# Kernel tuning notes

Measured on AMD Instinct MI355X. Metric: run time of the kernel, lower is better.

## Reference

```python
import jax, jax.numpy as jnp
import numpy as np

T, N, G, H, COV, TW, E = 96, 1024, 128, 512, 8, 8, 32768
D2 = TW * (TW - 1)          # 56, GNN summary width
IN = COV + D2               # 64, exogenous input width


def setup_inputs() -> dict:
    key = jax.random.key(0)
    ks = jax.random.split(key, 32)
    s = 1.0 / np.sqrt(H)

    def u(k, shape):
        return jax.random.uniform(k, shape, jnp.float32, -s, s)

    inp = {
        "input": jax.random.normal(ks[0], (T, 1, IN), jnp.float32),
        "x_nodes": jax.random.normal(ks[1], (T, N, N), jnp.float32),
        "edge_index": jax.random.randint(ks[2], (T, 2, E), 0, N, dtype=jnp.int64),
        "W1": u(ks[3], (N, G)), "b1": u(ks[4], (G,)),
        "W2": u(ks[5], (G, G)), "b2": u(ks[6], (G,)),
        "Wfc": u(ks[7], (G * N, D2)), "bfc": u(ks[8], (D2,)),
        "W_ii": u(ks[9], (IN, H)), "W_gi": u(ks[10], (D2, H)), "W_hi": u(ks[11], (H, H)), "b_i": u(ks[12], (H,)),
        "W_if": u(ks[13], (IN, H)), "W_gf": u(ks[14], (D2, H)), "W_hf": u(ks[15], (H, H)), "b_f": u(ks[16], (H,)),
        "W_ig": u(ks[17], (IN, H)), "W_gg": u(ks[18], (D2, H)), "W_hg": u(ks[19], (H, H)), "b_g": u(ks[20], (H,)),
        "W_io": u(ks[21], (IN, H)), "W_go": u(ks[22], (D2, H)), "W_ho": u(ks[23], (H, H)), "b_o": u(ks[24], (H,)),
    }
    return inp


def reference(input, x_nodes, edge_index,
              W1, b1, W2, b2, Wfc, bfc,
              W_ii, W_gi, W_hi, b_i,
              W_if, W_gf, W_hf, b_f,
              W_ig, W_gg, W_hg, b_g,
              W_io, W_go, W_ho, b_o):
    self_loops = jnp.arange(N, dtype=edge_index.dtype)

    def gcn_conv(x, src, dst, dinv, W, b):
        # GCNConv: out[dst] += d^-1/2[src] d^-1/2[dst] * (x @ W)[src], plus bias
        xw = x @ W                                   # [N, F_out]
        norm = dinv[src] * dinv[dst]                 # [E+N]
        msg = xw[src] * norm[:, None]
        return jax.ops.segment_sum(msg, dst, num_segments=N) + b

    def step(carry, inputs):
        h, c = carry
        x_t, xg, ei = inputs                         # [1,IN], [N,N], [2,E]
        src = jnp.concatenate([ei[0], self_loops])   # add self-loops
        dst = jnp.concatenate([ei[1], self_loops])
        deg = jax.ops.segment_sum(jnp.ones(src.shape, jnp.float32), dst, num_segments=N)
        dinv = jnp.where(deg > 0, jax.lax.rsqrt(jnp.maximum(deg, 1.0)), 0.0)

        xh = jax.nn.relu(gcn_conv(xg, src, dst, dinv, W1, b1))
        xh = gcn_conv(xh, src, dst, dinv, W2, b2)    # [N, G]
        g = jax.nn.relu(xh.reshape(1, -1) @ Wfc + bfc)  # [1, D2]

        i = jax.nn.sigmoid(x_t @ W_ii + g @ W_gi + h @ W_hi + b_i)
        f = jax.nn.sigmoid(x_t @ W_if + g @ W_gf + h @ W_hf + b_f)
        gt = jnp.tanh(x_t @ W_ig + g @ W_gg + h @ W_hg + b_g)
        o = jax.nn.sigmoid(x_t @ W_io + g @ W_go + h @ W_ho + b_o)
        c = f * c + i * gt
        h = o * jnp.tanh(c)
        return (h, c), h

    h0 = jnp.zeros((1, H), jnp.float32)
    c0 = jnp.zeros((1, H), jnp.float32)
    (h, c), outputs = jax.lax.scan(step, (h0, c0), (input, x_nodes, edge_index))
    return outputs, h, c
```

## Files before the change

### kernel.cpp

```cpp
#include <hip/hip_runtime.h>
#include <stdint.h>

#define T_    96
#define TC_   32
#define N_    1024
#define G_    128
#define H_    512
#define E_    32768
#define EN_   33792
#define D2_   56
#define IN_   64
#define KFC_  131072

typedef __bf16 bf16_t;
typedef __bf16 bf16x8 __attribute__((ext_vector_type(8)));
typedef float  f32x4  __attribute__((ext_vector_type(4)));
typedef unsigned short u16;
typedef unsigned long long u64;

struct PtrQuadF { const float* p[4]; };

__device__ inline bf16x8 cvt8(const float* p) {
    const f32x4 a0 = *(const f32x4*)p;
    const f32x4 a1 = *(const f32x4*)(p + 4);
    bf16x8 r;
    r[0] = (bf16_t)a0[0]; r[1] = (bf16_t)a0[1]; r[2] = (bf16_t)a0[2]; r[3] = (bf16_t)a0[3];
    r[4] = (bf16_t)a1[0]; r[5] = (bf16_t)a1[1]; r[6] = (bf16_t)a1[2]; r[7] = (bf16_t)a1[3];
    return r;
}


__global__ __launch_bounds__(256) void deg_kernel(const int* __restrict__ ei, int* __restrict__ deg) {
    int t = blockIdx.y;
    int idx = blockIdx.x * 256 + threadIdx.x;
    if (idx >= EN_) return;
    int d = (idx < E_) ? ei[(size_t)t * 2 * E_ + E_ + idx] : (idx - E_);
    atomicAdd(&deg[t * N_ + d], 1);
}

__global__ __launch_bounds__(1024) void scan_kernel(const int* __restrict__ deg, int* __restrict__ rowptr,
                                                    int* __restrict__ fill, float* __restrict__ dinv) {
    int t = blockIdx.x, i = threadIdx.x;
    __shared__ int a[N_], b[N_];
    int d = deg[t * N_ + i];
    a[i] = d;
    __syncthreads();
    int* cur = a; int* nxt = b;
    for (int off = 1; off < N_; off <<= 1) {
        int v = cur[i];
        if (i >= off) v += cur[i - off];
        nxt[i] = v;
        __syncthreads();
        int* tmp = cur; cur = nxt; nxt = tmp;
    }
    int incl = cur[i];
    int start = incl - d + t * EN_;
    rowptr[t * N_ + i] = start;
    fill[t * N_ + i] = start;
    dinv[t * N_ + i] = rsqrtf((float)d);
}

__global__ __launch_bounds__(256) void fill_kernel(const int* __restrict__ ei, int* __restrict__ fill,
                                                   u16* __restrict__ colv) {
    int t = blockIdx.y;
    int idx = blockIdx.x * 256 + threadIdx.x;
    if (idx >= EN_) return;
    int s, d;
    if (idx < E_) {
        s = ei[(size_t)t * 2 * E_ + idx];
        d = ei[(size_t)t * 2 * E_ + E_ + idx];
    } else {
        s = d = idx - E_;
    }
    int pos = atomicAdd(&fill[t * N_ + d], 1);
    colv[pos] = (u16)s;
}


__global__ __launch_bounds__(256) void densify_kernel(const int* __restrict__ rowptr, const int* __restrict__ deg,
                                                      const u16* __restrict__ colv, const float* __restrict__ dinv,
                                                      bf16_t* __restrict__ S, int t0) {
    int tl = blockIdx.y;
    int t = t0 + tl;
    int w = threadIdx.x >> 6, l = threadIdx.x & 63;
    int r = blockIdx.x * 4 + w;
    __shared__ float rowbuf[4][N_];
    for (int i = l; i < N_; i += 64) rowbuf[w][i] = 0.f;
    __syncthreads();
    int start = rowptr[t * N_ + r];
    int n = deg[t * N_ + r];
    float dr = dinv[t * N_ + r];
    for (int e = l; e < n; e += 64) {
        int c = colv[start + e];
        atomicAdd(&rowbuf[w][c], dinv[t * N_ + c] * dr);
    }
    __syncthreads();
    bf16_t* dst = S + ((size_t)tl * N_ + r) * N_;
    for (int i = l; i < N_; i += 64) dst[i] = (bf16_t)rowbuf[w][i];
}


__global__ __launch_bounds__(256) void transpose_kernel(const float* __restrict__ src, bf16_t* __restrict__ dst,
                                                        int R, int C, int Cpad) {
    __shared__ bf16_t tile[64][65];
    int rb = blockIdx.x * 64, cb = blockIdx.y * 64;
    int tx = threadIdx.x & 63, ty = threadIdx.x >> 6;
#pragma unroll
    for (int i = 0; i < 16; i++) {
        int r = rb + ty * 16 + i;
        int c = cb + tx;
        float v = 0.f;
        if (r < R && c < C) v = src[(size_t)r * C + c];
        tile[ty * 16 + i][tx] = (bf16_t)v;
    }
    __syncthreads();
#pragma unroll
    for (int i = 0; i < 16; i++) {
        int c = cb + ty * 16 + i;
        int r = rb + tx;
        if (c < Cpad && r < R) dst[(size_t)c * R + r] = tile[tx][ty * 16 + i];
    }
}


__global__ __launch_bounds__(256) void whcvt_kernel(PtrQuadF Wh, bf16_t* __restrict__ dst) {
    int g = blockIdx.y;
    int idx = blockIdx.x * 256 + threadIdx.x;
    dst[(size_t)g * H_ * H_ + idx] = (bf16_t)Wh.p[g][idx];
}


template<bool BF32>
__global__ __launch_bounds__(256) void gemm_g(const bf16_t* __restrict__ A, const void* __restrict__ Bp,
                                              bf16_t* __restrict__ C, const float* __restrict__ bias, int relu,
                                              int K, int Mtiles, size_t sA, size_t sB, size_t sC, int ldc) {
    int t = blockIdx.y;
    int mi = blockIdx.x % Mtiles, ni = blockIdx.x / Mtiles;
    int tid = threadIdx.x;
    int w = tid >> 6, l = tid & 63;
    int wm = w & 1, wn = w >> 1;
    int lm = l & 15, lq = l >> 4;
    f32x4 acc[4][4] = {};
    const bf16_t* Ab = A + sA * t + (size_t)(mi * 128 + wm * 64 + lm) * K + lq * 8;
    size_t bO = sB * t + (size_t)(ni * 128 + wn * 64 + lm) * K + lq * 8;
    const bf16_t* Bb16 = (const bf16_t*)Bp + bO;
    const float*  Bb32 = (const float*)Bp + bO;
    for (int k0 = 0; k0 < K; k0 += 32) {
        bf16x8 af[4], bfv[4];
#pragma unroll
        for (int i = 0; i < 4; i++) af[i] = *(const bf16x8*)(Ab + (size_t)i * 16 * K + k0);
#pragma unroll
        for (int i = 0; i < 4; i++) {
            if (BF32) bfv[i] = cvt8(Bb32 + (size_t)i * 16 * K + k0);
            else      bfv[i] = *(const bf16x8*)(Bb16 + (size_t)i * 16 * K + k0);
        }
#pragma unroll
        for (int mt = 0; mt < 4; mt++)
#pragma unroll
            for (int nt = 0; nt < 4; nt++)
                acc[mt][nt] = __builtin_amdgcn_mfma_f32_16x16x32_bf16(af[mt], bfv[nt], acc[mt][nt], 0, 0, 0);
    }
#pragma unroll
    for (int mt = 0; mt < 4; mt++)
#pragma unroll
        for (int nt = 0; nt < 4; nt++) {
            int colg = ni * 128 + wn * 64 + nt * 16 + lm;
            float bv = bias ? bias[colg] : 0.f;
#pragma unroll
            for (int r = 0; r < 4; r++) {
                int row = mi * 128 + wm * 64 + mt * 16 + lq * 4 + r;
                float v = acc[mt][nt][r] + bv;
                if (relu) v = fmaxf(v, 0.f);
                C[sC * t + (size_t)row * ldc + colg] = (bf16_t)v;
            }
        }
}


__global__ __launch_bounds__(256) void gfc_kernel(const bf16_t* __restrict__ XH2, const bf16_t* __restrict__ WfcT,
                                                  float* __restrict__ g_acc, int t0) {
    int tid = threadIdx.x;
    int w = tid >> 6, l = tid & 63;
    int lm = l & 15, lq = l >> 4;
    int n = w * 16 + lm;
    size_t k0 = (size_t)blockIdx.x * 1024;
    f32x4 acc[2] = {};
    const bf16_t* Ab = XH2 + (size_t)lm * KFC_ + k0 + lq * 8;
    const bf16_t* Bb = WfcT + (size_t)n * KFC_ + k0 + lq * 8;
    for (int ks = 0; ks < 32; ks++) {
        bf16x8 bfr = *(const bf16x8*)(Bb + ks * 32);
        bf16x8 a0  = *(const bf16x8*)(Ab + ks * 32);
        bf16x8 a1  = *(const bf16x8*)(Ab + (size_t)16 * KFC_ + ks * 32);
        acc[0] = __builtin_amdgcn_mfma_f32_16x16x32_bf16(a0, bfr, acc[0], 0, 0, 0);
        acc[1] = __builtin_amdgcn_mfma_f32_16x16x32_bf16(a1, bfr, acc[1], 0, 0, 0);
    }
#pragma unroll
    for (int mt = 0; mt < 2; mt++)
#pragma unroll
        for (int r = 0; r < 4; r++) {
            int t = t0 + mt * 16 + lq * 4 + r;
            if (n < D2_) atomicAdd(&g_acc[t * 64 + n], acc[mt][r]);
        }
}


__global__ __launch_bounds__(512) void pregate_kernel(const float* __restrict__ xin, const float* __restrict__ g_acc,
                                                      const float* __restrict__ bfc,
                                                      PtrQuadF Wi, PtrQuadF Wg, PtrQuadF Wb,
                                                      float* __restrict__ out) {
    int gate = blockIdx.x, t = blockIdx.y, j = threadIdx.x;
    __shared__ float gl[D2_];
    __shared__ float xl[IN_];
    if (j < D2_) gl[j] = fmaxf(g_acc[t * 64 + j] + bfc[j], 0.f);
    if (j < IN_) xl[j] = xin[t * IN_ + j];
    __syncthreads();
    const float* wi = Wi.p[gate];
    const float* wg = Wg.p[gate];
    float acc = Wb.p[gate][j];
#pragma unroll 4
    for (int k = 0; k < IN_; k++) acc += xl[k] * wi[k * H_ + j];
#pragma unroll 4
    for (int k = 0; k < D2_; k++) acc += gl[k] * wg[k * H_ + j];
    out[(t * 4 + gate) * H_ + j] = acc;
}


__global__ __launch_bounds__(256) void lstm_kernel(const bf16_t* __restrict__ Whb, const float* __restrict__ pregate,
                                                   u64* __restrict__ h_slot, float* __restrict__ out) {
    int tid = threadIdx.x, bid = blockIdx.x;
    int jl = tid >> 3, kc = tid & 7;
    int j = bid * 32 + jl;
    int k0 = kc * 64;

    uint32_t w[128];
#pragma unroll
    for (int g4 = 0; g4 < 4; g4++) {
        const bf16_t* W = Whb + (size_t)g4 * H_ * H_;
#pragma unroll
        for (int m = 0; m < 32; m++) {
            int k = k0 + 2 * m;
            uint32_t lo = *(const u16*)(W + (size_t)k * H_ + j);
            uint32_t hi = *(const u16*)(W + (size_t)(k + 1) * H_ + j);
            w[g4 * 32 + m] = lo | (hi << 16);
        }
    }

    __shared__ __align__(16) float hl[H_];
    hl[tid] = 0.f;
    hl[tid + 256] = 0.f;
    float c = 0.f;
    __syncthreads();

    for (int step = 0; step < 96; step++) {
        float p0 = 0.f, p1 = 0.f, p2 = 0.f, p3 = 0.f;
        if (kc == 0) {
            const float* pre = pregate + (size_t)step * (4 * H_);
            p0 = pre[0 * H_ + j]; p1 = pre[1 * H_ + j];
            p2 = pre[2 * H_ + j]; p3 = pre[3 * H_ + j];
        }

        float s0 = 0.f, s1 = 0.f, s2 = 0.f, s3 = 0.f;
        const float4* h4 = (const float4*)(hl + k0);
#pragma unroll
        for (int q = 0; q < 16; q++) {
            float4 hq = h4[q];
#pragma unroll
            for (int p = 0; p < 2; p++) {
                float h0 = p ? hq.z : hq.x;
                float h1 = p ? hq.w : hq.y;
                int mi = q * 2 + p;
                uint32_t wv;
                wv = w[0 * 32 + mi];
                s0 += __uint_as_float(wv << 16) * h0 + __uint_as_float(wv & 0xffff0000u) * h1;
                wv = w[1 * 32 + mi];
                s1 += __uint_as_float(wv << 16) * h0 + __uint_as_float(wv & 0xffff0000u) * h1;
                wv = w[2 * 32 + mi];
                s2 += __uint_as_float(wv << 16) * h0 + __uint_as_float(wv & 0xffff0000u) * h1;
                wv = w[3 * 32 + mi];
                s3 += __uint_as_float(wv << 16) * h0 + __uint_as_float(wv & 0xffff0000u) * h1;
            }
        }
        s0 += __shfl_xor(s0, 1); s0 += __shfl_xor(s0, 2); s0 += __shfl_xor(s0, 4);
        s1 += __shfl_xor(s1, 1); s1 += __shfl_xor(s1, 2); s1 += __shfl_xor(s1, 4);
        s2 += __shfl_xor(s2, 1); s2 += __shfl_xor(s2, 2); s2 += __shfl_xor(s2, 4);
        s3 += __shfl_xor(s3, 1); s3 += __shfl_xor(s3, 2); s3 += __shfl_xor(s3, 4);

        if (kc == 0) {
            float ig = 1.f / (1.f + __expf(-(s0 + p0)));
            float fg = 1.f / (1.f + __expf(-(s1 + p1)));
            float gg = tanhf(s2 + p2);
            float og = 1.f / (1.f + __expf(-(s3 + p3)));
            c = fg * c + ig * gg;
            float h = og * tanhf(c);
            if (step < 95) {
                u64 v = ((u64)(unsigned int)(step + 1) << 32) | (u64)__float_as_uint(h);
                __hip_atomic_store(&h_slot[(size_t)step * H_ + j], v, __ATOMIC_RELAXED, __HIP_MEMORY_SCOPE_AGENT);
            }
            out[step * H_ + j] = h;
            if (step == 95) {
                out[96 * H_ + j] = h;
                out[97 * H_ + j] = c;
            }
        }
        if (step < 95) {
            __syncthreads();
            if (tid < 64) {
                unsigned int want = (unsigned int)(step + 1);
                const u64* base = h_slot + (size_t)step * H_ + tid * 8;
                u64 v[8];
                int need = 0xff;
                while (need) {
#pragma unroll
                    for (int s = 0; s < 8; s++)
                        if (need & (1 << s))
                            v[s] = __hip_atomic_load(&base[s], __ATOMIC_RELAXED, __HIP_MEMORY_SCOPE_AGENT);
                    int nd = 0;
#pragma unroll
                    for (int s = 0; s < 8; s++)
                        if ((need & (1 << s)) && (unsigned int)(v[s] >> 32) != want) nd |= 1 << s;
                    need = nd;
                    if (need) __builtin_amdgcn_s_sleep(1);
                }
                float4 f0, f1;
                f0.x = __uint_as_float((unsigned int)v[0]); f0.y = __uint_as_float((unsigned int)v[1]);
                f0.z = __uint_as_float((unsigned int)v[2]); f0.w = __uint_as_float((unsigned int)v[3]);
                f1.x = __uint_as_float((unsigned int)v[4]); f1.y = __uint_as_float((unsigned int)v[5]);
                f1.z = __uint_as_float((unsigned int)v[6]); f1.w = __uint_as_float((unsigned int)v[7]);
                ((float4*)hl)[tid * 2] = f0;
                ((float4*)hl)[tid * 2 + 1] = f1;
            }
            __syncthreads();
        }
    }
}


extern "C" void kernel_launch(void* const* d_in, const int* in_sizes, int n_in,
                              void* d_out, int out_size, void* d_ws, size_t ws_size,
                              hipStream_t stream) {
    const float* xin    = (const float*)d_in[0];
    const float* xnodes = (const float*)d_in[1];
    const int*   ei     = (const int*)d_in[2];
    const float* W1  = (const float*)d_in[3];
    const float* b1  = (const float*)d_in[4];
    const float* W2  = (const float*)d_in[5];
    const float* b2  = (const float*)d_in[6];
    const float* Wfc = (const float*)d_in[7];
    const float* bfc = (const float*)d_in[8];

    PtrQuadF Wi = {{(const float*)d_in[9],  (const float*)d_in[13], (const float*)d_in[17], (const float*)d_in[21]}};
    PtrQuadF Wg = {{(const float*)d_in[10], (const float*)d_in[14], (const float*)d_in[18], (const float*)d_in[22]}};
    PtrQuadF Wh = {{(const float*)d_in[11], (const float*)d_in[15], (const float*)d_in[19], (const float*)d_in[23]}};
    PtrQuadF Wb = {{(const float*)d_in[12], (const float*)d_in[16], (const float*)d_in[20], (const float*)d_in[24]}};

    char* ws = (char*)d_ws;
    size_t off = 0;
    auto alloc = [&](size_t bytes) { void* p = ws + off; off += (bytes + 255) & ~(size_t)255; return p; };

    bf16_t* S       = (bf16_t*)alloc((size_t)TC_ * N_ * N_ * 2);
    bf16_t* C1T     = (bf16_t*)alloc((size_t)TC_ * 128 * N_ * 2);
    bf16_t* XH1     = (bf16_t*)alloc((size_t)TC_ * N_ * 128 * 2);
    bf16_t* C2T     = (bf16_t*)alloc((size_t)TC_ * 128 * N_ * 2);
    u16*    colv    = (u16*)   alloc((size_t)T_ * EN_ * 2);
    int*    deg     = (int*)   alloc((size_t)T_ * N_ * 4);
    int*    rowptr  = (int*)   alloc((size_t)T_ * N_ * 4);
    int*    fillp   = (int*)   alloc((size_t)T_ * N_ * 4);
    float*  dinv    = (float*) alloc((size_t)T_ * N_ * 4);
    bf16_t* W1t     = (bf16_t*)alloc((size_t)128 * 1024 * 2);
    bf16_t* W2t     = (bf16_t*)alloc((size_t)128 * 128 * 2);
    bf16_t* WfcT    = (bf16_t*)alloc((size_t)64 * KFC_ * 2);
    bf16_t* Whb     = (bf16_t*)alloc((size_t)4 * H_ * H_ * 2);
    float*  g_acc   = (float*) alloc((size_t)T_ * 64 * 4);
    float*  pregate = (float*) alloc((size_t)T_ * 4 * H_ * 4);
    u64*    h_slot  = (u64*)   alloc((size_t)T_ * H_ * 8);
    bf16_t* XH2     = C1T;

    hipMemsetAsync(deg, 0, (size_t)T_ * N_ * 4, stream);
    hipMemsetAsync(g_acc, 0, (size_t)T_ * 64 * 4, stream);

    deg_kernel<<<dim3(132, T_), 256, 0, stream>>>(ei, deg);
    scan_kernel<<<T_, 1024, 0, stream>>>(deg, rowptr, fillp, dinv);
    fill_kernel<<<dim3(132, T_), 256, 0, stream>>>(ei, fillp, colv);

    transpose_kernel<<<dim3(16, 2), 256, 0, stream>>>(W1, W1t, 1024, 128, 128);
    transpose_kernel<<<dim3(2, 2), 256, 0, stream>>>(W2, W2t, 128, 128, 128);
    transpose_kernel<<<dim3(2048, 1), 256, 0, stream>>>(Wfc, WfcT, KFC_, D2_, 64);
    whcvt_kernel<<<dim3(1024, 4), 256, 0, stream>>>(Wh, Whb);

    for (int c = 0; c < T_ / TC_; c++) {
        int t0 = c * TC_;
        densify_kernel<<<dim3(256, TC_), 256, 0, stream>>>(rowptr, deg, colv, dinv, S, t0);
        gemm_g<true><<<dim3(8, TC_), 256, 0, stream>>>(
            W1t, xnodes + (size_t)t0 * N_ * N_, C1T, nullptr, 0,
            1024, 1, 0, (size_t)N_ * N_, (size_t)128 * N_, N_);
        gemm_g<false><<<dim3(8, TC_), 256, 0, stream>>>(
            S, C1T, XH1, b1, 1,
            1024, 8, (size_t)N_ * N_, (size_t)128 * N_, (size_t)N_ * 128, 128);
        gemm_g<false><<<dim3(8, TC_), 256, 0, stream>>>(
            W2t, XH1, C2T, nullptr, 0,
            128, 1, 0, (size_t)N_ * 128, (size_t)128 * N_, N_);
        gemm_g<false><<<dim3(8, TC_), 256, 0, stream>>>(
            S, C2T, XH2, b2, 0,
            1024, 8, (size_t)N_ * N_, (size_t)128 * N_, (size_t)N_ * 128, 128);
        gfc_kernel<<<128, 256, 0, stream>>>(XH2, WfcT, g_acc, t0);
    }

    pregate_kernel<<<dim3(4, T_), 512, 0, stream>>>(xin, g_acc, bfc, Wi, Wg, Wb, pregate);

    lstm_kernel<<<16, 256, 0, stream>>>(Whb, pregate, h_slot, (float*)d_out);
}
```

Measured before the change: 1.622 ms.

## Replace dense normalized adjacency GEMMs with CSR sparse aggregation

```diff
diff --git a/kernel.cpp b/kernel.cpp
--- a/kernel.cpp
+++ b/kernel.cpp
@@ -61,7 +61,7 @@
 }
 
 __global__ __launch_bounds__(256) void fill_kernel(const int* __restrict__ ei, int* __restrict__ fill,
-                                                   u16* __restrict__ colv) {
+                                                   const float* __restrict__ dinv, u64* __restrict__ ecv) {
     int t = blockIdx.y;
     int idx = blockIdx.x * 256 + threadIdx.x;
     if (idx >= EN_) return;
@@ -72,31 +72,9 @@
     } else {
         s = d = idx - E_;
     }
+    float nrm = dinv[t * N_ + s] * dinv[t * N_ + d];
     int pos = atomicAdd(&fill[t * N_ + d], 1);
-    colv[pos] = (u16)s;
-}
-
-
-__global__ __launch_bounds__(256) void densify_kernel(const int* __restrict__ rowptr, const int* __restrict__ deg,
-                                                      const u16* __restrict__ colv, const float* __restrict__ dinv,
-                                                      bf16_t* __restrict__ S, int t0) {
-    int tl = blockIdx.y;
-    int t = t0 + tl;
-    int w = threadIdx.x >> 6, l = threadIdx.x & 63;
-    int r = blockIdx.x * 4 + w;
-    __shared__ float rowbuf[4][N_];
-    for (int i = l; i < N_; i += 64) rowbuf[w][i] = 0.f;
-    __syncthreads();
-    int start = rowptr[t * N_ + r];
-    int n = deg[t * N_ + r];
-    float dr = dinv[t * N_ + r];
-    for (int e = l; e < n; e += 64) {
-        int c = colv[start + e];
-        atomicAdd(&rowbuf[w][c], dinv[t * N_ + c] * dr);
-    }
-    __syncthreads();
-    bf16_t* dst = S + ((size_t)tl * N_ + r) * N_;
-    for (int i = l; i < N_; i += 64) dst[i] = (bf16_t)rowbuf[w][i];
+    ecv[pos] = ((u64)__float_as_uint(nrm) << 32) | (unsigned int)s;
 }
 
 
@@ -120,6 +98,23 @@
         int r = rb + tx;
         if (c < Cpad && r < R) dst[(size_t)c * R + r] = tile[tx][ty * 16 + i];
     }
+}
+
+
+__global__ __launch_bounds__(256) void transpose16_kernel(const bf16_t* __restrict__ src, bf16_t* __restrict__ dst) {
+    __shared__ bf16_t tile[64][65];
+    int tl = blockIdx.z;
+    const bf16_t* s = src + (size_t)tl * 128 * N_;
+    bf16_t* d = dst + (size_t)tl * N_ * 128;
+    int rb = blockIdx.y * 64, cb = blockIdx.x * 64;
+    int tx = threadIdx.x & 63, ty = threadIdx.x >> 6;
+#pragma unroll
+    for (int i = 0; i < 16; i++)
+        tile[ty * 16 + i][tx] = s[(size_t)(rb + ty * 16 + i) * N_ + cb + tx];
+    __syncthreads();
+#pragma unroll
+    for (int i = 0; i < 16; i++)
+        d[(size_t)(cb + ty * 16 + i) * 128 + rb + tx] = tile[tx][ty * 16 + i];
 }
 
 
@@ -174,6 +169,43 @@
                 C[sC * t + (size_t)row * ldc + colg] = (bf16_t)v;
             }
         }
+}
+
+
+__device__ inline void spmm_acc(u64 q, const bf16_t* Fb, int l, float& a0, float& a1) {
+    int c = (int)(unsigned int)q;
+    float wn = __uint_as_float((unsigned int)(q >> 32));
+    unsigned int pk = *(const unsigned int*)(Fb + (size_t)c * 128 + 2 * l);
+    a0 += wn * __uint_as_float(pk << 16);
+    a1 += wn * __uint_as_float(pk & 0xffff0000u);
+}
+
+__global__ __launch_bounds__(256) void spmm_kernel(const int* __restrict__ rowptr, const int* __restrict__ deg,
+                                                   const u64* __restrict__ ecv, const bf16_t* __restrict__ F,
+                                                   const float* __restrict__ bias, int relu,
+                                                   bf16_t* __restrict__ out, int t0) {
+    int tl = blockIdx.y, t = t0 + tl;
+    int w = threadIdx.x >> 6, l = threadIdx.x & 63;
+    int r = blockIdx.x * 4 + w;
+    int start = rowptr[t * N_ + r];
+    int n = deg[t * N_ + r];
+    const bf16_t* Fb = F + (size_t)tl * N_ * 128;
+    const u64* ep = ecv + start;
+    float a0 = 0.f, a1 = 0.f;
+    int e = 0;
+    for (; e + 4 <= n; e += 4) {
+        u64 q0 = ep[e], q1 = ep[e + 1], q2 = ep[e + 2], q3 = ep[e + 3];
+        spmm_acc(q0, Fb, l, a0, a1);
+        spmm_acc(q1, Fb, l, a0, a1);
+        spmm_acc(q2, Fb, l, a0, a1);
+        spmm_acc(q3, Fb, l, a0, a1);
+    }
+    for (; e < n; e++) spmm_acc(ep[e], Fb, l, a0, a1);
+    float v0 = a0 + bias[2 * l], v1 = a1 + bias[2 * l + 1];
+    if (relu) { v0 = fmaxf(v0, 0.f); v1 = fmaxf(v1, 0.f); }
+    bf16_t b0 = (bf16_t)v0, b1 = (bf16_t)v1;
+    unsigned int po = (unsigned int)*(u16*)&b0 | ((unsigned int)*(u16*)&b1 << 16);
+    *(unsigned int*)((u16*)(out + ((size_t)tl * N_ + r) * 128) + 2 * l) = po;
 }
 
 
@@ -357,11 +389,12 @@
     size_t off = 0;
     auto alloc = [&](size_t bytes) { void* p = ws + off; off += (bytes + 255) & ~(size_t)255; return p; };
 
-    bf16_t* S       = (bf16_t*)alloc((size_t)TC_ * N_ * N_ * 2);
     bf16_t* C1T     = (bf16_t*)alloc((size_t)TC_ * 128 * N_ * 2);
+    bf16_t* C1      = (bf16_t*)alloc((size_t)TC_ * N_ * 128 * 2);
     bf16_t* XH1     = (bf16_t*)alloc((size_t)TC_ * N_ * 128 * 2);
-    bf16_t* C2T     = (bf16_t*)alloc((size_t)TC_ * 128 * N_ * 2);
-    u16*    colv    = (u16*)   alloc((size_t)T_ * EN_ * 2);
+    bf16_t* C2      = (bf16_t*)alloc((size_t)TC_ * N_ * 128 * 2);
+    bf16_t* XH2     = (bf16_t*)alloc((size_t)TC_ * N_ * 128 * 2);
+    u64*    ecv     = (u64*)   alloc((size_t)T_ * EN_ * 8);
     int*    deg     = (int*)   alloc((size_t)T_ * N_ * 4);
     int*    rowptr  = (int*)   alloc((size_t)T_ * N_ * 4);
     int*    fillp   = (int*)   alloc((size_t)T_ * N_ * 4);
@@ -373,14 +406,13 @@
     float*  g_acc   = (float*) alloc((size_t)T_ * 64 * 4);
     float*  pregate = (float*) alloc((size_t)T_ * 4 * H_ * 4);
     u64*    h_slot  = (u64*)   alloc((size_t)T_ * H_ * 8);
-    bf16_t* XH2     = C1T;
 
     hipMemsetAsync(deg, 0, (size_t)T_ * N_ * 4, stream);
     hipMemsetAsync(g_acc, 0, (size_t)T_ * 64 * 4, stream);
 
     deg_kernel<<<dim3(132, T_), 256, 0, stream>>>(ei, deg);
     scan_kernel<<<T_, 1024, 0, stream>>>(deg, rowptr, fillp, dinv);
-    fill_kernel<<<dim3(132, T_), 256, 0, stream>>>(ei, fillp, colv);
+    fill_kernel<<<dim3(132, T_), 256, 0, stream>>>(ei, fillp, dinv, ecv);
 
     transpose_kernel<<<dim3(16, 2), 256, 0, stream>>>(W1, W1t, 1024, 128, 128);
     transpose_kernel<<<dim3(2, 2), 256, 0, stream>>>(W2, W2t, 128, 128, 128);
@@ -389,19 +421,15 @@
 
     for (int c = 0; c < T_ / TC_; c++) {
         int t0 = c * TC_;
-        densify_kernel<<<dim3(256, TC_), 256, 0, stream>>>(rowptr, deg, colv, dinv, S, t0);
         gemm_g<true><<<dim3(8, TC_), 256, 0, stream>>>(
             W1t, xnodes + (size_t)t0 * N_ * N_, C1T, nullptr, 0,
             1024, 1, 0, (size_t)N_ * N_, (size_t)128 * N_, N_);
+        transpose16_kernel<<<dim3(16, 2, TC_), 256, 0, stream>>>(C1T, C1);
+        spmm_kernel<<<dim3(256, TC_), 256, 0, stream>>>(rowptr, deg, ecv, C1, b1, 1, XH1, t0);
         gemm_g<false><<<dim3(8, TC_), 256, 0, stream>>>(
-            S, C1T, XH1, b1, 1,
-            1024, 8, (size_t)N_ * N_, (size_t)128 * N_, (size_t)N_ * 128, 128);
-        gemm_g<false><<<dim3(8, TC_), 256, 0, stream>>>(
-            W2t, XH1, C2T, nullptr, 0,
-            128, 1, 0, (size_t)N_ * 128, (size_t)128 * N_, N_);
-        gemm_g<false><<<dim3(8, TC_), 256, 0, stream>>>(
-            S, C2T, XH2, b2, 0,
-            1024, 8, (size_t)N_ * N_, (size_t)128 * N_, (size_t)N_ * 128, 128);
+            XH1, W2t, C2, nullptr, 0,
+            128, 8, (size_t)N_ * 128, 0, (size_t)N_ * 128, 128);
+        spmm_kernel<<<dim3(256, TC_), 256, 0, stream>>>(rowptr, deg, ecv, C2, b2, 0, XH2, t0);
         gfc_kernel<<<128, 256, 0, stream>>>(XH2, WfcT, g_acc, t0);
     }
 
```

New measurement: 1.587 ms. 1.02x faster.
